# Optimization experiments

Hardware: AMD Instinct MI355X
Metric: run time of the kernel (lower is better)

The kernel has to match this reference:

```python
import jax, jax.numpy as jnp
import numpy as np

N_NODES = 100000
N_EDGES = 800000
IN_FEATS = 128
OUT_FEATS = 128
RANK_DIM = 128
NUM_BOND_TYPES = 32


def setup_inputs() -> dict:
    key = jax.random.key(0)
    ks = jax.random.split(key, 8)
    feat = jax.random.normal(ks[0], (N_NODES, IN_FEATS), dtype=jnp.float32)
    src = jax.random.randint(ks[1], (N_EDGES,), 0, N_NODES)
    dst = jax.random.randint(ks[2], (N_EDGES,), 0, N_NODES)
    # guarantee every node has in-degree >= 1 (module forbids 0-in-degree nodes)
    dst = dst.at[:N_NODES].set(jnp.arange(N_NODES))
    edge_attr = jax.random.randint(ks[3], (N_EDGES,), 0, NUM_BOND_TYPES)
    # xavier-uniform-like params
    def xavier(k, shape):
        lim = float(np.sqrt(6.0 / (shape[0] + shape[1])))
        return jax.random.uniform(k, shape, jnp.float32, -lim, lim)
    w1 = xavier(ks[4], (IN_FEATS, OUT_FEATS))
    w2 = xavier(ks[5], (IN_FEATS + 1, RANK_DIM))
    v = xavier(ks[6], (RANK_DIM, OUT_FEATS))
    bond_emb = jax.random.normal(ks[7], (NUM_BOND_TYPES, OUT_FEATS), dtype=jnp.float32)
    return {"feat": feat, "src": src, "dst": dst, "edge_attr": edge_attr,
            "w1": w1, "w2": w2, "v": v, "bond_emb": bond_emb}


def reference(feat, src, dst, edge_attr, w1, w2, v, bond_emb):
    N = feat.shape[0]
    E = src.shape[0]
    ones_e = jnp.ones((E,), dtype=feat.dtype)
    # norm == 'both': scale source features by out_degree^{-1/2}
    out_deg = jnp.clip(jax.ops.segment_sum(ones_e, src, num_segments=N), 1.0)
    feat_src = feat * (out_deg ** -0.5)[:, None]
    # two small GEMMs on node features
    h_sum = feat_src @ w1  # [N, out]
    feat_aug = jnp.concatenate([feat_src, jnp.ones((N, 1), dtype=feat.dtype)], axis=1)
    h_prod = jnp.tanh(feat_aug @ w2)  # [N, rank]
    # edge embedding (BondEncoder)
    ew = bond_emb[edge_attr]  # [E, out]
    # u_mul_e then neighbor-wise product / sum reductions onto dst
    m_prod = h_prod[src] * ew
    m_sum = h_sum[src] * ew
    hp = jax.ops.segment_prod(m_prod, dst, num_segments=N)
    hs = jax.ops.segment_sum(m_sum, dst, num_segments=N)
    rst = hs + hp @ v
    # norm == 'both': scale result by in_degree^{-1/2}
    in_deg = jnp.clip(jax.ops.segment_sum(ones_e, dst, num_segments=N), 1.0)
    rst = rst * (in_deg ** -0.5)[:, None]
    return rst
```

## Files before the change

### kernel.cpp

```cpp
#include <hip/hip_runtime.h>

#define N_NODES 100000
#define N_EDGES 800000

typedef unsigned short u16;
typedef unsigned int u32;
typedef __attribute__((ext_vector_type(8))) short short8;
typedef __attribute__((ext_vector_type(4))) float floatx4;

#define NBUK 196
#define BSH 9
#define NBLK 256
#define NE4 (N_EDGES / 4)
#define CE 782
#define NB_PREPW 192

__device__ __forceinline__ float bflo(u32 u) {
    union { u32 i; float f; } v; v.i = u << 16; return v.f;
}
__device__ __forceinline__ float bfhi(u32 u) {
    union { u32 i; float f; } v; v.i = u & 0xFFFF0000u; return v.f;
}
__device__ __forceinline__ u16 f2bf(float f) {
    union { float f; u32 i; } v; v.f = f;
    u32 r = (v.i + 0x7FFFu + ((v.i >> 16) & 1u)) >> 16;
    return (u16)r;
}
__device__ __forceinline__ float fast_tanh(float x) {
    float e = __expf(2.0f * x);
    return 1.0f - 2.0f * __builtin_amdgcn_rcpf(e + 1.0f);
}


__global__ __launch_bounds__(256) void kA_count(const int* __restrict__ src, const int* __restrict__ dst,
                                                int* __restrict__ countsD, int* __restrict__ countsS,
                                                const float* __restrict__ w1, const float* __restrict__ w2,
                                                const float* __restrict__ v, u16* __restrict__ wvfrag) {
    __shared__ int cd[NBUK], cs[NBUK];
    if (blockIdx.x >= NBLK) {
        int idx = (blockIdx.x - NBLK) * 256 + threadIdx.x;
        if (idx < 3 * 16384) {
            int m = idx >> 14, r = idx & 16383;
            int k = r >> 7, o = r & 127;
            float val = (m == 0) ? w1[k * 128 + o] : (m == 1) ? w2[k * 128 + o] : v[k * 128 + o];
            int ot = o >> 4, ks = k >> 5, quad = (k >> 3) & 3, j = k & 7;
            int lane = (quad << 4) | (o & 15);
            wvfrag[(((m * 8 + ot) * 4 + ks) * 64 + lane) * 8 + j] = f2bf(val);
        }
        return;
    }
    for (int i = threadIdx.x; i < NBUK; i += 256) { cd[i] = 0; cs[i] = 0; }
    __syncthreads();
    int i0 = blockIdx.x * CE;
    int i1 = i0 + CE; if (i1 > NE4) i1 = NE4;
    for (int i = i0 + threadIdx.x; i < i1; i += 256) {
        int4 d4 = ((const int4*)dst)[i];
        int4 s4 = ((const int4*)src)[i];
        atomicAdd(&cd[d4.x >> BSH], 1); atomicAdd(&cd[d4.y >> BSH], 1);
        atomicAdd(&cd[d4.z >> BSH], 1); atomicAdd(&cd[d4.w >> BSH], 1);
        atomicAdd(&cs[s4.x >> BSH], 1); atomicAdd(&cs[s4.y >> BSH], 1);
        atomicAdd(&cs[s4.z >> BSH], 1); atomicAdd(&cs[s4.w >> BSH], 1);
    }
    __syncthreads();
    for (int i = threadIdx.x; i < NBUK; i += 256) {
        countsD[i * NBLK + blockIdx.x] = cd[i];
        countsS[i * NBLK + blockIdx.x] = cs[i];
    }
}


__global__ __launch_bounds__(256) void kA_scan(int* __restrict__ countsD, int* __restrict__ countsS,
                                               int* __restrict__ totD, int* __restrict__ totS) {
    __shared__ int sc[256];
    int b = blockIdx.x;
    int* cnt = (b < NBUK) ? (countsD + b * NBLK) : (countsS + (b - NBUK) * NBLK);
    int t = threadIdx.x;
    int v0 = cnt[t];
    sc[t] = v0; __syncthreads();
    for (int off = 1; off < 256; off <<= 1) {
        int x = (t >= off) ? sc[t - off] : 0;
        __syncthreads();
        sc[t] += x;
        __syncthreads();
    }
    cnt[t] = sc[t] - v0;
    if (t == 255) { if (b < NBUK) totD[b] = sc[255]; else totS[b - NBUK] = sc[255]; }
}


__global__ __launch_bounds__(256) void kA_scatter(const int* __restrict__ src, const int* __restrict__ dst,
                                                  const int* __restrict__ attr,
                                                  const int* __restrict__ countsD, const int* __restrict__ countsS,
                                                  const int* __restrict__ totD, const int* __restrict__ totS,
                                                  u32* __restrict__ dbuf, u16* __restrict__ sbuf) {
    __shared__ int curD[NBUK], curS[NBUK];
    __shared__ int sd[256], ss[256];
    int t = threadIdx.x;
    int vd = (t < NBUK) ? totD[t] : 0;
    int vs = (t < NBUK) ? totS[t] : 0;
    sd[t] = vd; ss[t] = vs; __syncthreads();
    for (int off = 1; off < 256; off <<= 1) {
        int xd = (t >= off) ? sd[t - off] : 0;
        int xs = (t >= off) ? ss[t - off] : 0;
        __syncthreads();
        sd[t] += xd; ss[t] += xs;
        __syncthreads();
    }
    if (t < NBUK) {
        curD[t] = (sd[t] - vd) + countsD[t * NBLK + blockIdx.x];
        curS[t] = (ss[t] - vs) + countsS[t * NBLK + blockIdx.x];
    }
    __syncthreads();
    int i0 = blockIdx.x * CE;
    int i1 = i0 + CE; if (i1 > NE4) i1 = NE4;
    for (int i = i0 + t; i < i1; i += 256) {
        int4 s4 = ((const int4*)src)[i];
        int4 d4 = ((const int4*)dst)[i];
        int4 a4 = ((const int4*)attr)[i];
        int p, d, s, a;
        d = d4.x; s = s4.x; a = a4.x;
        p = atomicAdd(&curD[d >> BSH], 1);
        dbuf[p] = ((u32)(d & 511) << 22) | ((u32)s << 5) | (u32)a;
        p = atomicAdd(&curS[s >> BSH], 1); sbuf[p] = (u16)(s & 511);
        d = d4.y; s = s4.y; a = a4.y;
        p = atomicAdd(&curD[d >> BSH], 1);
        dbuf[p] = ((u32)(d & 511) << 22) | ((u32)s << 5) | (u32)a;
        p = atomicAdd(&curS[s >> BSH], 1); sbuf[p] = (u16)(s & 511);
        d = d4.z; s = s4.z; a = a4.z;
        p = atomicAdd(&curD[d >> BSH], 1);
        dbuf[p] = ((u32)(d & 511) << 22) | ((u32)s << 5) | (u32)a;
        p = atomicAdd(&curS[s >> BSH], 1); sbuf[p] = (u16)(s & 511);
        d = d4.w; s = s4.w; a = a4.w;
        p = atomicAdd(&curD[d >> BSH], 1);
        dbuf[p] = ((u32)(d & 511) << 22) | ((u32)s << 5) | (u32)a;
        p = atomicAdd(&curS[s >> BSH], 1); sbuf[p] = (u16)(s & 511);
    }
}


__global__ __launch_bounds__(256) void k_build(const u32* __restrict__ dbuf, const u16* __restrict__ sbuf,
                                               const int* __restrict__ totD, const int* __restrict__ totS,
                                               int* __restrict__ csr_start, int* __restrict__ in_deg,
                                               float* __restrict__ in_scale, float* __restrict__ out_scale,
                                               int* __restrict__ csr_edge) {
    __shared__ int cnt[512];
    __shared__ int aux[512];
    __shared__ int sc[256];
    __shared__ int sbase;
    int t = threadIdx.x;
    int isS = blockIdx.x >= NBUK;
    int b = isS ? (blockIdx.x - NBUK) : blockIdx.x;
    const int* tot = isS ? totS : totD;
    if (t < 64) {
        int s = 0;
        for (int i = t; i < b; i += 64) s += tot[i];
#pragma unroll
        for (int o = 32; o > 0; o >>= 1) s += __shfl_down(s, o);
        if (t == 0) sbase = s;
    }
    for (int i = t; i < 512; i += 256) cnt[i] = 0;
    __syncthreads();
    int st = sbase, n = tot[b];
    int nb0 = b << BSH;
    if (isS) {
        for (int i = st + t; i < st + n; i += 256) atomicAdd(&cnt[sbuf[i]], 1);
        __syncthreads();
        for (int s2 = t; s2 < 512; s2 += 256) {
            int node = nb0 + s2;
            if (node < N_NODES) { int c = cnt[s2]; if (c < 1) c = 1; out_scale[node] = rsqrtf((float)c); }
        }
        return;
    }
    for (int i = st + t; i < st + n; i += 256) { u32 r = dbuf[i]; atomicAdd(&cnt[r >> 22], 1); }
    __syncthreads();
    int c0 = cnt[2 * t], c1 = cnt[2 * t + 1];
    int s = c0 + c1; sc[t] = s; __syncthreads();
    for (int off = 1; off < 256; off <<= 1) {
        int x = (t >= off) ? sc[t - off] : 0;
        __syncthreads();
        sc[t] += x;
        __syncthreads();
    }
    int excl = sc[t] - s;
    aux[2 * t] = excl; aux[2 * t + 1] = excl + c0;
    int na = nb0 + 2 * t, nbv = nb0 + 2 * t + 1;
    if (na < N_NODES) {
        in_deg[na] = c0; int cc = c0 < 1 ? 1 : c0;
        in_scale[na] = rsqrtf((float)cc); csr_start[na] = st + excl;
    }
    if (nbv < N_NODES) {
        in_deg[nbv] = c1; int cc = c1 < 1 ? 1 : c1;
        in_scale[nbv] = rsqrtf((float)cc); csr_start[nbv] = st + excl + c0;
    }
    __syncthreads();
    for (int i = st + t; i < st + n; i += 256) {
        u32 r = dbuf[i];
        int pos = atomicAdd(&aux[r >> 22], 1);
        csr_edge[st + pos] = (int)(r & 0x3FFFFFu);
    }
}


__global__ __launch_bounds__(256) void k_gemm(const float* __restrict__ feat,
                                              const float* __restrict__ out_scale,
                                              const u16* __restrict__ wvfrag,
                                              const float* __restrict__ w2,
                                              u16* __restrict__ hrow) {
    int wave = threadIdx.x >> 6, lane = threadIdx.x & 63;
    int quad = lane >> 4, l15 = lane & 15;
    const float* bias = w2 + 128 * 128;
    float bias_v[8];
#pragma unroll
    for (int ot = 0; ot < 8; ot++) bias_v[ot] = bias[ot * 16 + l15];
    const short8* wv = (const short8*)wvfrag;
    int nb = blockIdx.x * 64 + wave * 16;
    int anode = nb + l15; if (anode >= N_NODES) anode = N_NODES - 1;
    float s = out_scale[anode];
    short8 a[4];
#pragma unroll
    for (int ks = 0; ks < 4; ks++) {
        float4 f0 = *(const float4*)(feat + anode * 128 + ks * 32 + quad * 8);
        float4 f1 = *(const float4*)(feat + anode * 128 + ks * 32 + quad * 8 + 4);
        short8 av;
        av[0] = (short)f2bf(f0.x * s); av[1] = (short)f2bf(f0.y * s);
        av[2] = (short)f2bf(f0.z * s); av[3] = (short)f2bf(f0.w * s);
        av[4] = (short)f2bf(f1.x * s); av[5] = (short)f2bf(f1.y * s);
        av[6] = (short)f2bf(f1.z * s); av[7] = (short)f2bf(f1.w * s);
        a[ks] = av;
    }
#pragma unroll
    for (int ot = 0; ot < 8; ot++) {
        floatx4 accS = (floatx4){0.f, 0.f, 0.f, 0.f};
        floatx4 accP = (floatx4){0.f, 0.f, 0.f, 0.f};
#pragma unroll
        for (int ks = 0; ks < 4; ks++) {
            short8 b0 = wv[(ot * 4 + ks) * 64 + lane];
            short8 b1 = wv[((8 + ot) * 4 + ks) * 64 + lane];
            accS = __builtin_amdgcn_mfma_f32_16x16x32_bf16(a[ks], b0, accS, 0, 0, 0);
            accP = __builtin_amdgcn_mfma_f32_16x16x32_bf16(a[ks], b1, accP, 0, 0, 0);
        }
        int o = ot * 16 + l15;
#pragma unroll
        for (int r = 0; r < 4; r++) {
            int node = nb + quad * 4 + r;
            if (node < N_NODES) {
                u32 pv = (u32)f2bf(accS[r]) | ((u32)f2bf(fast_tanh(accP[r] + bias_v[ot])) << 16);
                *(u32*)(hrow + node * 256 + o * 2) = pv;
            }
        }
    }
}


__global__ __launch_bounds__(256, 8) void k_edge(const int* __restrict__ csr_start, const int* __restrict__ in_deg,
                                                 const int* __restrict__ csr_edge,
                                                 const u16* __restrict__ hrow,
                                                 const float* __restrict__ bond_emb,
                                                 float* __restrict__ out_hs, u16* __restrict__ hp) {
    int wid = (blockIdx.x * 256 + threadIdx.x) >> 6;
    int lane = threadIdx.x & 63;
    int nwaves = (gridDim.x * 256) >> 6;
    const int NPAIR = N_NODES / 2;
    uint2 hC0 = {0, 0}, hC1 = {0, 0};
    float2 eC0 = {0.f, 0.f}, eC1 = {0.f, 0.f};
    for (int pr = wid; pr < NPAIR; pr += nwaves) {
        int n0 = pr * 2, n1 = n0 + 1;
        int st0 = csr_start[n0];
        int2 dd = *(const int2*)(in_deg + n0);
        int d0 = dd.x, d1 = dd.y;
        int st1 = st0 + d0;
        float as0 = 0.f, as1 = 0.f, ap0 = 1.f, ap1 = 1.f;
        float bs0 = 0.f, bs1 = 0.f, bp0 = 1.f, bp1 = 1.f;
        int b0 = 0, b1 = 0;
        while (b0 < d0 || b1 < d1) {
            int c0 = d0 - b0; c0 = c0 < 0 ? 0 : (c0 > 64 ? 64 : c0);
            int c1 = d1 - b1; c1 = c1 < 0 ? 0 : (c1 > 64 ? 64 : c1);
            int pkv0 = 0, pkv1 = 0;
            if (c0 > 0) { int li = lane < c0 ? lane : c0 - 1; pkv0 = csr_edge[st0 + b0 + li]; }
            if (c1 > 0) { int li = lane < c1 ? lane : c1 - 1; pkv1 = csr_edge[st1 + b1 + li]; }
            uint2 hA0 = hC0, hB0 = hC0, hA1 = hC1, hB1 = hC1;
            float2 eA0 = eC0, eB0 = eC0, eA1 = eC1, eB1 = eC1;
            if (c0 > 0) {
                int pk = __builtin_amdgcn_readlane(pkv0, 0);
                hA0 = *(const uint2*)(hrow + (pk >> 5) * 256 + 4 * lane);
                eA0 = *(const float2*)(bond_emb + (pk & 31) * 128 + 2 * lane);
                if (c0 > 1) {
                    pk = __builtin_amdgcn_readlane(pkv0, 1);
                    hB0 = *(const uint2*)(hrow + (pk >> 5) * 256 + 4 * lane);
                    eB0 = *(const float2*)(bond_emb + (pk & 31) * 128 + 2 * lane);
                }
            }
            if (c1 > 0) {
                int pk = __builtin_amdgcn_readlane(pkv1, 0);
                hA1 = *(const uint2*)(hrow + (pk >> 5) * 256 + 4 * lane);
                eA1 = *(const float2*)(bond_emb + (pk & 31) * 128 + 2 * lane);
                if (c1 > 1) {
                    pk = __builtin_amdgcn_readlane(pkv1, 1);
                    hB1 = *(const uint2*)(hrow + (pk >> 5) * 256 + 4 * lane);
                    eB1 = *(const float2*)(bond_emb + (pk & 31) * 128 + 2 * lane);
                }
            }
            int cm = c0 > c1 ? c0 : c1;
            for (int j = 0; j < cm; j++) {
                int jn = j + 2;
                if (jn < c0) {
                    int pk = __builtin_amdgcn_readlane(pkv0, jn);
                    hC0 = *(const uint2*)(hrow + (pk >> 5) * 256 + 4 * lane);
                    eC0 = *(const float2*)(bond_emb + (pk & 31) * 128 + 2 * lane);
                }
                if (jn < c1) {
                    int pk = __builtin_amdgcn_readlane(pkv1, jn);
                    hC1 = *(const uint2*)(hrow + (pk >> 5) * 256 + 4 * lane);
                    eC1 = *(const float2*)(bond_emb + (pk & 31) * 128 + 2 * lane);
                }
                if (j < c0) {
                    as0 += bflo(hA0.x) * eA0.x;
                    ap0 *= bfhi(hA0.x) * eA0.x;
                    as1 += bflo(hA0.y) * eA0.y;
                    ap1 *= bfhi(hA0.y) * eA0.y;
                    hA0 = hB0; eA0 = eB0; hB0 = hC0; eB0 = eC0;
                }
                if (j < c1) {
                    bs0 += bflo(hA1.x) * eA1.x;
                    bp0 *= bfhi(hA1.x) * eA1.x;
                    bs1 += bflo(hA1.y) * eA1.y;
                    bp1 *= bfhi(hA1.y) * eA1.y;
                    hA1 = hB1; eA1 = eB1; hB1 = hC1; eB1 = eC1;
                }
            }
            b0 += 64; b1 += 64;
        }
        float2 sv0; sv0.x = as0; sv0.y = as1;
        float2 sv1; sv1.x = bs0; sv1.y = bs1;
        *(float2*)(out_hs + n0 * 128 + 2 * lane) = sv0;
        *(float2*)(out_hs + n1 * 128 + 2 * lane) = sv1;
        *(u32*)(hp + n0 * 128 + 2 * lane) = ((u32)f2bf(ap1) << 16) | (u32)f2bf(ap0);
        *(u32*)(hp + n1 * 128 + 2 * lane) = ((u32)f2bf(bp1) << 16) | (u32)f2bf(bp0);
    }
}


__global__ __launch_bounds__(256) void k_final(const u16* __restrict__ hp,
                                               const u16* __restrict__ vfrag,
                                               const float* __restrict__ in_scale,
                                               float* __restrict__ out) {
    int wave = threadIdx.x >> 6, lane = threadIdx.x & 63;
    int quad = lane >> 4, l15 = lane & 15;
    const short8* wv = (const short8*)vfrag;
    int nb = blockIdx.x * 64 + wave * 16;
    int anode = nb + l15; if (anode >= N_NODES) anode = N_NODES - 1;
    short8 a[4];
#pragma unroll
    for (int ks = 0; ks < 4; ks++)
        a[ks] = *(const short8*)(hp + anode * 128 + ks * 32 + quad * 8);
#pragma unroll
    for (int ot = 0; ot < 8; ot++) {
        floatx4 acc = (floatx4){0.f, 0.f, 0.f, 0.f};
#pragma unroll
        for (int ks = 0; ks < 4; ks++) {
            short8 b = wv[(ot * 4 + ks) * 64 + lane];
            acc = __builtin_amdgcn_mfma_f32_16x16x32_bf16(a[ks], b, acc, 0, 0, 0);
        }
        int o = ot * 16 + l15;
#pragma unroll
        for (int r = 0; r < 4; r++) {
            int node = nb + quad * 4 + r;
            if (node < N_NODES) {
                float scl = in_scale[node];
                float hsv = out[node * 128 + o];
                out[node * 128 + o] = (acc[r] + hsv) * scl;
            }
        }
    }
}

extern "C" void kernel_launch(void* const* d_in, const int* in_sizes, int n_in,
                              void* d_out, int out_size, void* d_ws, size_t ws_size,
                              hipStream_t stream) {
    const float* feat = (const float*)d_in[0];
    const int* src = (const int*)d_in[1];
    const int* dst = (const int*)d_in[2];
    const int* attr = (const int*)d_in[3];
    const float* w1 = (const float*)d_in[4];
    const float* w2 = (const float*)d_in[5];
    const float* v = (const float*)d_in[6];
    const float* bond = (const float*)d_in[7];
    float* out = (float*)d_out;

    char* ws = (char*)d_ws;
    size_t off = 0;
    auto alloc = [&](size_t bytes) -> char* {
        char* p = ws + off; off += (bytes + 255) & ~(size_t)255; return p;
    };
    int* countsD   = (int*)alloc((size_t)NBUK * NBLK * 4);
    int* countsS   = (int*)alloc((size_t)NBUK * NBLK * 4);
    int* totD      = (int*)alloc((size_t)NBUK * 4);
    int* totS      = (int*)alloc((size_t)NBUK * 4);
    u32* dbuf      = (u32*)alloc((size_t)N_EDGES * 4);
    u16* sbuf      = (u16*)alloc((size_t)N_EDGES * 2);
    int* csr_start = (int*)alloc((size_t)N_NODES * 4);
    int* in_deg    = (int*)alloc((size_t)N_NODES * 4);
    float* out_scale = (float*)alloc((size_t)N_NODES * 4);
    float* in_scale  = (float*)alloc((size_t)N_NODES * 4);
    int* csr_edge  = (int*)alloc((size_t)N_EDGES * 4);
    u16* wvfrag = (u16*)alloc((size_t)3 * 16384 * 2);
    u16* hrow   = (u16*)alloc((size_t)N_NODES * 256 * 2);
    u16* hp     = (u16*)alloc((size_t)N_NODES * 128 * 2);

    (void)in_sizes; (void)n_in; (void)out_size; (void)ws_size;

    kA_count<<<NBLK + NB_PREPW, 256, 0, stream>>>(src, dst, countsD, countsS, w1, w2, v, wvfrag);
    kA_scan<<<2 * NBUK, 256, 0, stream>>>(countsD, countsS, totD, totS);
    kA_scatter<<<NBLK, 256, 0, stream>>>(src, dst, attr, countsD, countsS, totD, totS, dbuf, sbuf);
    k_build<<<2 * NBUK, 256, 0, stream>>>(dbuf, sbuf, totD, totS,
                                          csr_start, in_deg, in_scale, out_scale, csr_edge);
    k_gemm<<<(N_NODES + 63) / 64, 256, 0, stream>>>(feat, out_scale, wvfrag, w2, hrow);
    k_edge<<<2048, 256, 0, stream>>>(csr_start, in_deg, csr_edge, hrow, bond, out, hp);
    k_final<<<(N_NODES + 63) / 64, 256, 0, stream>>>(hp, wvfrag + 2 * 16384, in_scale, out);
}
```

Before: 265.1 us.

## Fuse CSR build stages into one cooperative kernel with grid syncs

Merges the four preprocessing kernels (count, scan, scatter, build) into one cooperative kernel launched with 256 blocks, using grid.sync between phases instead of separate launches. The intent is to remove the launch gaps and tail effects of four small kernels. In exchange the scan and build phases now run only 256 blocks, looping over 392 tasks, so each block does more serial work. The grid-wide barriers also carry their own cost.

Measured after the change: 456.9 us. +72.4%, slower.

```diff
diff --git a/kernel.cpp b/kernel.cpp
--- a/kernel.cpp
+++ b/kernel.cpp
@@ -1,4 +1,7 @@
 #include <hip/hip_runtime.h>
+#include <hip/hip_cooperative_groups.h>
+
+namespace cg = cooperative_groups;
 
 #define N_NODES 100000
 #define N_EDGES 800000
@@ -13,7 +16,6 @@
 #define NBLK 256
 #define NE4 (N_EDGES / 4)
 #define CE 782
-#define NB_PREPW 192
 
 __device__ __forceinline__ float bflo(u32 u) {
     union { u32 i; float f; } v; v.i = u << 16; return v.f;
@@ -32,13 +34,28 @@
 }
 
 
-__global__ __launch_bounds__(256) void kA_count(const int* __restrict__ src, const int* __restrict__ dst,
+__global__ __launch_bounds__(256) void kA_fused(const int* __restrict__ src, const int* __restrict__ dst,
+                                                const int* __restrict__ attr,
+                                                const float* __restrict__ w1, const float* __restrict__ w2,
+                                                const float* __restrict__ v, u16* __restrict__ wvfrag,
                                                 int* __restrict__ countsD, int* __restrict__ countsS,
-                                                const float* __restrict__ w1, const float* __restrict__ w2,
-                                                const float* __restrict__ v, u16* __restrict__ wvfrag) {
+                                                int* __restrict__ totD, int* __restrict__ totS,
+                                                u32* __restrict__ dbuf, u16* __restrict__ sbuf,
+                                                int* __restrict__ csr_start, int* __restrict__ in_deg,
+                                                float* __restrict__ in_scale, float* __restrict__ out_scale,
+                                                int* __restrict__ csr_edge) {
+    cg::grid_group grid = cg::this_grid();
     __shared__ int cd[NBUK], cs[NBUK];
-    if (blockIdx.x >= NBLK) {
-        int idx = (blockIdx.x - NBLK) * 256 + threadIdx.x;
+    __shared__ int sc[256];
+    __shared__ int curD[NBUK], curS[NBUK];
+    __shared__ int sd[256], ss[256];
+    __shared__ int cnt[512], aux[512];
+    __shared__ int sbase;
+    int bid = blockIdx.x;
+    int t = threadIdx.x;
+
+    {
+        int idx = bid * 256 + t;
         if (idx < 3 * 16384) {
             int m = idx >> 14, r = idx & 16383;
             int k = r >> 7, o = r & 127;
@@ -47,13 +64,12 @@
             int lane = (quad << 4) | (o & 15);
             wvfrag[(((m * 8 + ot) * 4 + ks) * 64 + lane) * 8 + j] = f2bf(val);
         }
-        return;
-    }
-    for (int i = threadIdx.x; i < NBUK; i += 256) { cd[i] = 0; cs[i] = 0; }
+    }
+    for (int i = t; i < NBUK; i += 256) { cd[i] = 0; cs[i] = 0; }
     __syncthreads();
-    int i0 = blockIdx.x * CE;
+    int i0 = bid * CE;
     int i1 = i0 + CE; if (i1 > NE4) i1 = NE4;
-    for (int i = i0 + threadIdx.x; i < i1; i += 256) {
+    for (int i = i0 + t; i < i1; i += 256) {
         int4 d4 = ((const int4*)dst)[i];
         int4 s4 = ((const int4*)src)[i];
         atomicAdd(&cd[d4.x >> BSH], 1); atomicAdd(&cd[d4.y >> BSH], 1);
@@ -62,141 +78,125 @@
         atomicAdd(&cs[s4.z >> BSH], 1); atomicAdd(&cs[s4.w >> BSH], 1);
     }
     __syncthreads();
-    for (int i = threadIdx.x; i < NBUK; i += 256) {
-        countsD[i * NBLK + blockIdx.x] = cd[i];
-        countsS[i * NBLK + blockIdx.x] = cs[i];
-    }
-}
-
-
-__global__ __launch_bounds__(256) void kA_scan(int* __restrict__ countsD, int* __restrict__ countsS,
-                                               int* __restrict__ totD, int* __restrict__ totS) {
-    __shared__ int sc[256];
-    int b = blockIdx.x;
-    int* cnt = (b < NBUK) ? (countsD + b * NBLK) : (countsS + (b - NBUK) * NBLK);
-    int t = threadIdx.x;
-    int v0 = cnt[t];
-    sc[t] = v0; __syncthreads();
-    for (int off = 1; off < 256; off <<= 1) {
-        int x = (t >= off) ? sc[t - off] : 0;
-        __syncthreads();
-        sc[t] += x;
-        __syncthreads();
-    }
-    cnt[t] = sc[t] - v0;
-    if (t == 255) { if (b < NBUK) totD[b] = sc[255]; else totS[b - NBUK] = sc[255]; }
-}
-
-
-__global__ __launch_bounds__(256) void kA_scatter(const int* __restrict__ src, const int* __restrict__ dst,
-                                                  const int* __restrict__ attr,
-                                                  const int* __restrict__ countsD, const int* __restrict__ countsS,
-                                                  const int* __restrict__ totD, const int* __restrict__ totS,
-                                                  u32* __restrict__ dbuf, u16* __restrict__ sbuf) {
-    __shared__ int curD[NBUK], curS[NBUK];
-    __shared__ int sd[256], ss[256];
-    int t = threadIdx.x;
-    int vd = (t < NBUK) ? totD[t] : 0;
-    int vs = (t < NBUK) ? totS[t] : 0;
-    sd[t] = vd; ss[t] = vs; __syncthreads();
-    for (int off = 1; off < 256; off <<= 1) {
-        int xd = (t >= off) ? sd[t - off] : 0;
-        int xs = (t >= off) ? ss[t - off] : 0;
-        __syncthreads();
-        sd[t] += xd; ss[t] += xs;
-        __syncthreads();
-    }
-    if (t < NBUK) {
-        curD[t] = (sd[t] - vd) + countsD[t * NBLK + blockIdx.x];
-        curS[t] = (ss[t] - vs) + countsS[t * NBLK + blockIdx.x];
-    }
-    __syncthreads();
-    int i0 = blockIdx.x * CE;
-    int i1 = i0 + CE; if (i1 > NE4) i1 = NE4;
-    for (int i = i0 + t; i < i1; i += 256) {
-        int4 s4 = ((const int4*)src)[i];
-        int4 d4 = ((const int4*)dst)[i];
-        int4 a4 = ((const int4*)attr)[i];
-        int p, d, s, a;
-        d = d4.x; s = s4.x; a = a4.x;
-        p = atomicAdd(&curD[d >> BSH], 1);
-        dbuf[p] = ((u32)(d & 511) << 22) | ((u32)s << 5) | (u32)a;
-        p = atomicAdd(&curS[s >> BSH], 1); sbuf[p] = (u16)(s & 511);
-        d = d4.y; s = s4.y; a = a4.y;
-        p = atomicAdd(&curD[d >> BSH], 1);
-        dbuf[p] = ((u32)(d & 511) << 22) | ((u32)s << 5) | (u32)a;
-        p = atomicAdd(&curS[s >> BSH], 1); sbuf[p] = (u16)(s & 511);
-        d = d4.z; s = s4.z; a = a4.z;
-        p = atomicAdd(&curD[d >> BSH], 1);
-        dbuf[p] = ((u32)(d & 511) << 22) | ((u32)s << 5) | (u32)a;
-        p = atomicAdd(&curS[s >> BSH], 1); sbuf[p] = (u16)(s & 511);
-        d = d4.w; s = s4.w; a = a4.w;
-        p = atomicAdd(&curD[d >> BSH], 1);
-        dbuf[p] = ((u32)(d & 511) << 22) | ((u32)s << 5) | (u32)a;
-        p = atomicAdd(&curS[s >> BSH], 1); sbuf[p] = (u16)(s & 511);
-    }
-}
-
-
-__global__ __launch_bounds__(256) void k_build(const u32* __restrict__ dbuf, const u16* __restrict__ sbuf,
-                                               const int* __restrict__ totD, const int* __restrict__ totS,
-                                               int* __restrict__ csr_start, int* __restrict__ in_deg,
-                                               float* __restrict__ in_scale, float* __restrict__ out_scale,
-                                               int* __restrict__ csr_edge) {
-    __shared__ int cnt[512];
-    __shared__ int aux[512];
-    __shared__ int sc[256];
-    __shared__ int sbase;
-    int t = threadIdx.x;
-    int isS = blockIdx.x >= NBUK;
-    int b = isS ? (blockIdx.x - NBUK) : blockIdx.x;
-    const int* tot = isS ? totS : totD;
-    if (t < 64) {
-        int s = 0;
-        for (int i = t; i < b; i += 64) s += tot[i];
-#pragma unroll
-        for (int o = 32; o > 0; o >>= 1) s += __shfl_down(s, o);
-        if (t == 0) sbase = s;
-    }
-    for (int i = t; i < 512; i += 256) cnt[i] = 0;
-    __syncthreads();
-    int st = sbase, n = tot[b];
-    int nb0 = b << BSH;
-    if (isS) {
-        for (int i = st + t; i < st + n; i += 256) atomicAdd(&cnt[sbuf[i]], 1);
-        __syncthreads();
-        for (int s2 = t; s2 < 512; s2 += 256) {
-            int node = nb0 + s2;
-            if (node < N_NODES) { int c = cnt[s2]; if (c < 1) c = 1; out_scale[node] = rsqrtf((float)c); }
-        }
-        return;
-    }
-    for (int i = st + t; i < st + n; i += 256) { u32 r = dbuf[i]; atomicAdd(&cnt[r >> 22], 1); }
-    __syncthreads();
-    int c0 = cnt[2 * t], c1 = cnt[2 * t + 1];
-    int s = c0 + c1; sc[t] = s; __syncthreads();
-    for (int off = 1; off < 256; off <<= 1) {
-        int x = (t >= off) ? sc[t - off] : 0;
-        __syncthreads();
-        sc[t] += x;
-        __syncthreads();
-    }
-    int excl = sc[t] - s;
-    aux[2 * t] = excl; aux[2 * t + 1] = excl + c0;
-    int na = nb0 + 2 * t, nbv = nb0 + 2 * t + 1;
-    if (na < N_NODES) {
-        in_deg[na] = c0; int cc = c0 < 1 ? 1 : c0;
-        in_scale[na] = rsqrtf((float)cc); csr_start[na] = st + excl;
-    }
-    if (nbv < N_NODES) {
-        in_deg[nbv] = c1; int cc = c1 < 1 ? 1 : c1;
-        in_scale[nbv] = rsqrtf((float)cc); csr_start[nbv] = st + excl + c0;
-    }
-    __syncthreads();
-    for (int i = st + t; i < st + n; i += 256) {
-        u32 r = dbuf[i];
-        int pos = atomicAdd(&aux[r >> 22], 1);
-        csr_edge[st + pos] = (int)(r & 0x3FFFFFu);
+    for (int i = t; i < NBUK; i += 256) {
+        countsD[i * NBLK + bid] = cd[i];
+        countsS[i * NBLK + bid] = cs[i];
+    }
+    __threadfence();
+    grid.sync();
+
+    for (int task = bid; task < 2 * NBUK; task += 256) {
+        int* cnt_row = (task < NBUK) ? (countsD + task * NBLK) : (countsS + (task - NBUK) * NBLK);
+        int v0 = cnt_row[t];
+        sc[t] = v0; __syncthreads();
+        for (int off = 1; off < 256; off <<= 1) {
+            int x = (t >= off) ? sc[t - off] : 0;
+            __syncthreads();
+            sc[t] += x;
+            __syncthreads();
+        }
+        cnt_row[t] = sc[t] - v0;
+        if (t == 255) { if (task < NBUK) totD[task] = sc[255]; else totS[task - NBUK] = sc[255]; }
+        __syncthreads();
+    }
+    __threadfence();
+    grid.sync();
+
+    {
+        int vd = (t < NBUK) ? totD[t] : 0;
+        int vs = (t < NBUK) ? totS[t] : 0;
+        sd[t] = vd; ss[t] = vs; __syncthreads();
+        for (int off = 1; off < 256; off <<= 1) {
+            int xd = (t >= off) ? sd[t - off] : 0;
+            int xs = (t >= off) ? ss[t - off] : 0;
+            __syncthreads();
+            sd[t] += xd; ss[t] += xs;
+            __syncthreads();
+        }
+        if (t < NBUK) {
+            curD[t] = (sd[t] - vd) + countsD[t * NBLK + bid];
+            curS[t] = (ss[t] - vs) + countsS[t * NBLK + bid];
+        }
+        __syncthreads();
+        for (int i = i0 + t; i < i1; i += 256) {
+            int4 s4 = ((const int4*)src)[i];
+            int4 d4 = ((const int4*)dst)[i];
+            int4 a4 = ((const int4*)attr)[i];
+            int p, d, s, a;
+            d = d4.x; s = s4.x; a = a4.x;
+            p = atomicAdd(&curD[d >> BSH], 1);
+            dbuf[p] = ((u32)(d & 511) << 22) | ((u32)s << 5) | (u32)a;
+            p = atomicAdd(&curS[s >> BSH], 1); sbuf[p] = (u16)(s & 511);
+            d = d4.y; s = s4.y; a = a4.y;
+            p = atomicAdd(&curD[d >> BSH], 1);
+            dbuf[p] = ((u32)(d & 511) << 22) | ((u32)s << 5) | (u32)a;
+            p = atomicAdd(&curS[s >> BSH], 1); sbuf[p] = (u16)(s & 511);
+            d = d4.z; s = s4.z; a = a4.z;
+            p = atomicAdd(&curD[d >> BSH], 1);
+            dbuf[p] = ((u32)(d & 511) << 22) | ((u32)s << 5) | (u32)a;
+            p = atomicAdd(&curS[s >> BSH], 1); sbuf[p] = (u16)(s & 511);
+            d = d4.w; s = s4.w; a = a4.w;
+            p = atomicAdd(&curD[d >> BSH], 1);
+            dbuf[p] = ((u32)(d & 511) << 22) | ((u32)s << 5) | (u32)a;
+            p = atomicAdd(&curS[s >> BSH], 1); sbuf[p] = (u16)(s & 511);
+        }
+    }
+    __threadfence();
+    grid.sync();
+
+    for (int task = bid; task < 2 * NBUK; task += 256) {
+        int isS = task >= NBUK;
+        int b = isS ? (task - NBUK) : task;
+        const int* tot = isS ? totS : totD;
+        if (t < 64) {
+            int s = 0;
+            for (int i = t; i < b; i += 64) s += tot[i];
+#pragma unroll
+            for (int o = 32; o > 0; o >>= 1) s += __shfl_down(s, o);
+            if (t == 0) sbase = s;
+        }
+        for (int i = t; i < 512; i += 256) cnt[i] = 0;
+        __syncthreads();
+        int st = sbase, n = tot[b];
+        int nb0 = b << BSH;
+        if (isS) {
+            for (int i = st + t; i < st + n; i += 256) atomicAdd(&cnt[sbuf[i]], 1);
+            __syncthreads();
+            for (int s2 = t; s2 < 512; s2 += 256) {
+                int node = nb0 + s2;
+                if (node < N_NODES) { int c = cnt[s2]; if (c < 1) c = 1; out_scale[node] = rsqrtf((float)c); }
+            }
+            __syncthreads();
+            continue;
+        }
+        for (int i = st + t; i < st + n; i += 256) { u32 r = dbuf[i]; atomicAdd(&cnt[r >> 22], 1); }
+        __syncthreads();
+        int c0 = cnt[2 * t], c1 = cnt[2 * t + 1];
+        int s = c0 + c1; sc[t] = s; __syncthreads();
+        for (int off = 1; off < 256; off <<= 1) {
+            int x = (t >= off) ? sc[t - off] : 0;
+            __syncthreads();
+            sc[t] += x;
+            __syncthreads();
+        }
+        int excl = sc[t] - s;
+        aux[2 * t] = excl; aux[2 * t + 1] = excl + c0;
+        int na = nb0 + 2 * t, nbv = nb0 + 2 * t + 1;
+        if (na < N_NODES) {
+            in_deg[na] = c0; int cc = c0 < 1 ? 1 : c0;
+            in_scale[na] = rsqrtf((float)cc); csr_start[na] = st + excl;
+        }
+        if (nbv < N_NODES) {
+            in_deg[nbv] = c1; int cc = c1 < 1 ? 1 : c1;
+            in_scale[nbv] = rsqrtf((float)cc); csr_start[nbv] = st + excl + c0;
+        }
+        __syncthreads();
+        for (int i = st + t; i < st + n; i += 256) {
+            u32 r = dbuf[i];
+            int pos = atomicAdd(&aux[r >> 22], 1);
+            csr_edge[st + pos] = (int)(r & 0x3FFFFFu);
+        }
+        __syncthreads();
     }
 }
 
@@ -409,11 +409,15 @@
 
     (void)in_sizes; (void)n_in; (void)out_size; (void)ws_size;
 
-    kA_count<<<NBLK + NB_PREPW, 256, 0, stream>>>(src, dst, countsD, countsS, w1, w2, v, wvfrag);
-    kA_scan<<<2 * NBUK, 256, 0, stream>>>(countsD, countsS, totD, totS);
-    kA_scatter<<<NBLK, 256, 0, stream>>>(src, dst, attr, countsD, countsS, totD, totS, dbuf, sbuf);
-    k_build<<<2 * NBUK, 256, 0, stream>>>(dbuf, sbuf, totD, totS,
-                                          csr_start, in_deg, in_scale, out_scale, csr_edge);
+    {
+        void* args[] = {(void*)&src, (void*)&dst, (void*)&attr,
+                        (void*)&w1, (void*)&w2, (void*)&v, (void*)&wvfrag,
+                        (void*)&countsD, (void*)&countsS, (void*)&totD, (void*)&totS,
+                        (void*)&dbuf, (void*)&sbuf,
+                        (void*)&csr_start, (void*)&in_deg, (void*)&in_scale, (void*)&out_scale,
+                        (void*)&csr_edge};
+        hipLaunchCooperativeKernel((void*)kA_fused, dim3(NBLK), dim3(256), args, 0, stream);
+    }
     k_gemm<<<(N_NODES + 63) / 64, 256, 0, stream>>>(feat, out_scale, wvfrag, w2, hrow);
     k_edge<<<2048, 256, 0, stream>>>(csr_start, in_deg, csr_edge, hrow, bond, out, hp);
     k_final<<<(N_NODES + 63) / 64, 256, 0, stream>>>(hp, wvfrag + 2 * 16384, in_scale, out);
```
